# Optimization experiments

Hardware: AMD Instinct MI355X
Metric: run time of the kernel (lower is better)

Reference implementation:

```python
import jax, jax.numpy as jnp
import numpy as np

B, S, IN_DIM, HID = 128, 512, 512, 1024


def setup_inputs() -> dict:
    key = jax.random.key(0)
    k0, k1, k2, k3, k4 = jax.random.split(key, 5)
    s_ih = 1.0 / np.sqrt(HID)
    return {
        "embedding_sequence": jax.random.normal(k0, (B, S, IN_DIM), dtype=jnp.float32),
        "w_ih": jax.random.uniform(k1, (3 * HID, IN_DIM), jnp.float32, -s_ih, s_ih),
        "w_hh": jax.random.uniform(k2, (3 * HID, HID), jnp.float32, -s_ih, s_ih),
        "b_ih": jax.random.uniform(k3, (3 * HID,), jnp.float32, -s_ih, s_ih),
        "b_hh": jax.random.uniform(k4, (3 * HID,), jnp.float32, -s_ih, s_ih),
    }


def _gru_scan(embedding_sequence, w_ih, w_hh, b_ih, b_hh):
    # Precompute input-side gate projections for all steps: [B,S,3H]
    gi_all = jnp.einsum('bsi,gi->bsg', embedding_sequence, w_ih) + b_ih

    def step(h, gi):
        gh = h @ w_hh.T + b_hh                      # [B,3H]
        i_r, i_z, i_n = jnp.split(gi, 3, axis=-1)
        h_r, h_z, h_n = jnp.split(gh, 3, axis=-1)
        r = jax.nn.sigmoid(i_r + h_r)
        z = jax.nn.sigmoid(i_z + h_z)
        n = jnp.tanh(i_n + r * h_n)
        h_new = (1.0 - z) * n + z * h
        return h_new, h_new

    h0 = jnp.zeros((embedding_sequence.shape[0], HID), dtype=embedding_sequence.dtype)
    h_last, hiddens = jax.lax.scan(step, h0, jnp.swapaxes(gi_all, 0, 1))
    return jnp.swapaxes(hiddens, 0, 1), h_last      # ([B,S,H], [B,H])


def reference(embedding_sequence, w_ih, w_hh, b_ih, b_hh):
    return _gru_scan(embedding_sequence, w_ih, w_hh, b_ih, b_hh)
```

## Files before the change

kernel.cpp:

```cpp
#include <hip/hip_runtime.h>
#include <hip/hip_bf16.h>

#define BB   128
#define SS   512
#define IND  512
#define HID  1024
#define NBLK 256
#define GRPBLK 64
#define NSTRIPE 8

#define WHH_LD (HID + 8)
#define WIH_LD (IND + 8)

typedef __attribute__((ext_vector_type(8))) short s8v;
typedef __attribute__((ext_vector_type(4))) float f4v;
typedef unsigned long long u64;
typedef unsigned int u32;

__device__ __forceinline__ short f2bf(float f) {
    union { float f; u32 u; } v; v.f = f;
    u32 u = v.u + 0x7FFFu + ((v.u >> 16) & 1u);
    return (short)(u >> 16);
}


__global__ void __launch_bounds__(128, 1)
gru_persistent(const float* __restrict__ X,
               const float* __restrict__ Wih,
               const float* __restrict__ Whh,
               const float* __restrict__ bih,
               const float* __restrict__ bhh,
               float* __restrict__ out,
               short* __restrict__ bufA,
               short* __restrict__ bufB,
               u64*   __restrict__ ctr)
{
    __shared__ __align__(16) short whh_lds[48 * WHH_LD];
    __shared__ __align__(16) short wih_lds[48 * WIH_LD];

    const int tid  = threadIdx.x;
    const int wave = tid >> 6;
    const int lane = tid & 63;
    const int blk  = blockIdx.x;
    const int mi   = blk >> 6;
    const int jg   = blk & 63;

    for (int idx = tid; idx < 48 * (HID / 4); idx += 128) {
        int s = idx / (HID / 4), k4 = idx % (HID / 4);
        int grow = (s >> 4) * HID + jg * 16 + (s & 15);
        float4 v = *(const float4*)(Whh + (size_t)grow * HID + k4 * 4);
        short* d = &whh_lds[s * WHH_LD + k4 * 4];
        d[0] = f2bf(v.x); d[1] = f2bf(v.y); d[2] = f2bf(v.z); d[3] = f2bf(v.w);
    }
    for (int idx = tid; idx < 48 * (IND / 4); idx += 128) {
        int s = idx / (IND / 4), k4 = idx % (IND / 4);
        int grow = (s >> 4) * HID + jg * 16 + (s & 15);
        float4 v = *(const float4*)(Wih + (size_t)grow * IND + k4 * 4);
        short* d = &wih_lds[s * WIH_LD + k4 * 4];
        d[0] = f2bf(v.x); d[1] = f2bf(v.y); d[2] = f2bf(v.z); d[3] = f2bf(v.w);
    }

    const int n  = lane & 15;
    const int kg = lane >> 4;
    const int j  = jg * 16 + n;
    const float bir = bih[j], biz = bih[HID + j], bin_ = bih[2 * HID + j];
    const float bhr = bhh[j], bhz = bhh[HID + j], bhn  = bhh[2 * HID + j];

    const int rowbase = mi * 32 + wave * 16;
    const int wg      = mi * 2 + wave;

    const int wkk = j >> 5, wkg = (j >> 3) & 3;
    const u32 rest   = (u32)wkk * 1024u + (u32)wkg * 256u
                     + (u32)kg * 64u + ((u32)(n & 7) << 1);
    const u32 wbyteA = (u32)wg * 32768u + rest;
    const u32 wbyteB = (u32)mi * 131072u + (u32)(wg & 1) * 32768u + rest;

    const u64* hbA = (const u64*)bufA + (size_t)wg * 4096 + lane * 2;
    const u64* hbB = (const u64*)bufB + (size_t)mi * 16384
                   + (size_t)(wg & 1) * 4096 + lane * 2;

    float hkeep[4] = {0.f, 0.f, 0.f, 0.f};

    __syncthreads();

    for (int t = 0; t < SS; ++t) {
        f4v acc_r  = {0.f,0.f,0.f,0.f};
        f4v acc_z  = {0.f,0.f,0.f,0.f};
        f4v acc_in = {0.f,0.f,0.f,0.f};
        f4v acc_hn = {0.f,0.f,0.f,0.f};

        {
            const float* xrow = X + ((size_t)(rowbase + n) * SS + t) * IND;
            #pragma unroll 4
            for (int kk = 0; kk < IND / 32; ++kk) {
                const int k0 = kk * 32 + kg * 8;
                const float4* px = (const float4*)(xrow + k0);
                float4 x0 = px[0], x1 = px[1];
                s8v a;
                a[0]=f2bf(x0.x); a[1]=f2bf(x0.y); a[2]=f2bf(x0.z); a[3]=f2bf(x0.w);
                a[4]=f2bf(x1.x); a[5]=f2bf(x1.y); a[6]=f2bf(x1.z); a[7]=f2bf(x1.w);
                s8v br = *(const s8v*)&wih_lds[(0 * 16 + n) * WIH_LD + k0];
                s8v bz = *(const s8v*)&wih_lds[(1 * 16 + n) * WIH_LD + k0];
                s8v bn = *(const s8v*)&wih_lds[(2 * 16 + n) * WIH_LD + k0];
                acc_r  = __builtin_amdgcn_mfma_f32_16x16x32_bf16(a, br, acc_r,  0,0,0);
                acc_z  = __builtin_amdgcn_mfma_f32_16x16x32_bf16(a, bz, acc_z,  0,0,0);
                acc_in = __builtin_amdgcn_mfma_f32_16x16x32_bf16(a, bn, acc_in, 0,0,0);
            }
        }

        if (t > 0) {
            const u64* hb = (t & 1) ? hbA : hbB;
            s8v areg[32];
            #pragma unroll
            for (int kk = 0; kk < 32; ++kk) {
                u64 lo = __hip_atomic_load(hb + kk * 128,
                                           __ATOMIC_RELAXED, __HIP_MEMORY_SCOPE_AGENT);
                u64 hi = __hip_atomic_load(hb + kk * 128 + 1,
                                           __ATOMIC_RELAXED, __HIP_MEMORY_SCOPE_AGENT);
                union { u64 q[2]; s8v v; } u; u.q[0] = lo; u.q[1] = hi;
                areg[kk] = u.v;
            }
            #pragma unroll
            for (int kk = 0; kk < 32; ++kk) {
                const int k0 = kk * 32 + kg * 8;
                s8v br = *(const s8v*)&whh_lds[(0 * 16 + n) * WHH_LD + k0];
                s8v bz = *(const s8v*)&whh_lds[(1 * 16 + n) * WHH_LD + k0];
                s8v bn = *(const s8v*)&whh_lds[(2 * 16 + n) * WHH_LD + k0];
                acc_r  = __builtin_amdgcn_mfma_f32_16x16x32_bf16(areg[kk], br, acc_r,  0,0,0);
                acc_z  = __builtin_amdgcn_mfma_f32_16x16x32_bf16(areg[kk], bz, acc_z,  0,0,0);
                acc_hn = __builtin_amdgcn_mfma_f32_16x16x32_bf16(areg[kk], bn, acc_hn, 0,0,0);
            }
        }

        u32 packv[4];
        #pragma unroll
        for (int r = 0; r < 4; ++r) {
            const int b = rowbase + kg * 4 + r;
            float gr = acc_r[r] + bir + bhr;
            float gz = acc_z[r] + biz + bhz;
            float rr = 1.f / (1.f + __expf(-gr));
            float zz = 1.f / (1.f + __expf(-gz));
            float hn = acc_hn[r] + bhn;
            float na = acc_in[r] + bin_ + rr * hn;
            float e2 = __expf(2.f * na);
            float nn = (e2 - 1.f) / (e2 + 1.f);
            float hnew = (1.f - zz) * nn + zz * hkeep[r];
            hkeep[r] = hnew;
            out[(size_t)b * (SS * HID) + (size_t)t * HID + j] = hnew;
            if (t == SS - 1)
                out[(size_t)BB * SS * HID + (size_t)b * HID + j] = hnew;
            u32 hb16  = (u32)(unsigned short)f2bf(hnew);
            u32 other = (u32)__shfl_xor((int)hb16, 1);
            packv[r] = hb16 | (other << 16);
        }

        if (t < SS - 1) {
            if (!(n & 1)) {
                char* base = (t & 1) ? ((char*)bufB + wbyteB) : ((char*)bufA + wbyteA);
                #pragma unroll
                for (int r = 0; r < 4; ++r)
                    __hip_atomic_store((u32*)(base + r * 16), packv[r],
                                       __ATOMIC_RELAXED, __HIP_MEMORY_SCOPE_AGENT);
            }
            __syncthreads();
            if (tid == 0) {
                __hip_atomic_fetch_add(&ctr[(mi * NSTRIPE + (blk & 7)) * 8], 1ull,
                                       __ATOMIC_RELAXED, __HIP_MEMORY_SCOPE_AGENT);
                const u64 target = (u64)GRPBLK * (u64)(t + 1);
                for (;;) {
                    u64 s = 0;
                    #pragma unroll
                    for (int i = 0; i < NSTRIPE; ++i)
                        s += __hip_atomic_load(&ctr[(mi * NSTRIPE + i) * 8],
                                               __ATOMIC_RELAXED,
                                               __HIP_MEMORY_SCOPE_AGENT);
                    if (s >= target) break;
                    __builtin_amdgcn_s_sleep(1);
                }
            }
            __syncthreads();
        }
    }
}

extern "C" void kernel_launch(void* const* d_in, const int* in_sizes, int n_in,
                              void* d_out, int out_size, void* d_ws, size_t ws_size,
                              hipStream_t stream) {
    const float* X   = (const float*)d_in[0];
    const float* Wih = (const float*)d_in[1];
    const float* Whh = (const float*)d_in[2];
    const float* bih = (const float*)d_in[3];
    const float* bhh = (const float*)d_in[4];
    float* out = (float*)d_out;

    u64*   ctr  = (u64*)d_ws;
    short* bufA = (short*)((char*)d_ws + 4096);
    short* bufB = (short*)(out + (size_t)BB * SS * HID);

    hipMemsetAsync(d_ws, 0, 4096, stream);

    void* args[] = { (void*)&X, (void*)&Wih, (void*)&Whh, (void*)&bih,
                     (void*)&bhh, (void*)&out, (void*)&bufA, (void*)&bufB,
                     (void*)&ctr };
    hipLaunchCooperativeKernel((const void*)gru_persistent,
                               dim3(NBLK), dim3(128), args, 0, stream);
}
```

Baseline: 4.069 ms.

## Split GRU gate matmuls across six waves with LDS reduction

The block grows from 2 to 6 waves, and each wave group handles one gate (r, z, n) instead of one wave computing all three. Gate results are gathered through a small LDS buffer, and wave group 0 applies the nonlinearity and publishes h. Hidden-state loads are also issued before the input projection so their latency is hidden. This shortens the serial MFMA chain per step on the recurrent critical path, at the cost of an extra block barrier, LDS traffic, and redundant h loads in three waves.

```diff
diff --git a/kernel.cpp b/kernel.cpp
--- a/kernel.cpp
+++ b/kernel.cpp
@@ -8,6 +8,7 @@
 #define NBLK 256
 #define GRPBLK 64
 #define NSTRIPE 8
+#define NTHR 384
 
 #define WHH_LD (HID + 8)
 #define WIH_LD (IND + 8)
@@ -24,7 +25,7 @@
 }
 
 
-__global__ void __launch_bounds__(128, 1)
+__global__ void __launch_bounds__(NTHR, 1)
 gru_persistent(const float* __restrict__ X,
                const float* __restrict__ Wih,
                const float* __restrict__ Whh,
@@ -37,6 +38,7 @@
 {
     __shared__ __align__(16) short whh_lds[48 * WHH_LD];
     __shared__ __align__(16) short wih_lds[48 * WIH_LD];
+    __shared__ __align__(16) f4v  red_lds[3][2][64];
 
     const int tid  = threadIdx.x;
     const int wave = tid >> 6;
@@ -45,14 +47,17 @@
     const int mi   = blk >> 6;
     const int jg   = blk & 63;
 
-    for (int idx = tid; idx < 48 * (HID / 4); idx += 128) {
+    const int g  = wave >> 1;
+    const int rw = wave & 1;
+
+    for (int idx = tid; idx < 48 * (HID / 4); idx += NTHR) {
         int s = idx / (HID / 4), k4 = idx % (HID / 4);
         int grow = (s >> 4) * HID + jg * 16 + (s & 15);
         float4 v = *(const float4*)(Whh + (size_t)grow * HID + k4 * 4);
         short* d = &whh_lds[s * WHH_LD + k4 * 4];
         d[0] = f2bf(v.x); d[1] = f2bf(v.y); d[2] = f2bf(v.z); d[3] = f2bf(v.w);
     }
-    for (int idx = tid; idx < 48 * (IND / 4); idx += 128) {
+    for (int idx = tid; idx < 48 * (IND / 4); idx += NTHR) {
         int s = idx / (IND / 4), k4 = idx % (IND / 4);
         int grow = (s >> 4) * HID + jg * 16 + (s & 15);
         float4 v = *(const float4*)(Wih + (size_t)grow * IND + k4 * 4);
@@ -66,8 +71,8 @@
     const float bir = bih[j], biz = bih[HID + j], bin_ = bih[2 * HID + j];
     const float bhr = bhh[j], bhz = bhh[HID + j], bhn  = bhh[2 * HID + j];
 
-    const int rowbase = mi * 32 + wave * 16;
-    const int wg      = mi * 2 + wave;
+    const int rowbase = mi * 32 + rw * 16;
+    const int wg      = mi * 2 + rw;
 
     const int wkk = j >> 5, wkg = (j >> 3) & 3;
     const u32 rest   = (u32)wkk * 1024u + (u32)wkg * 256u
@@ -84,10 +89,23 @@
     __syncthreads();
 
     for (int t = 0; t < SS; ++t) {
-        f4v acc_r  = {0.f,0.f,0.f,0.f};
-        f4v acc_z  = {0.f,0.f,0.f,0.f};
-        f4v acc_in = {0.f,0.f,0.f,0.f};
-        f4v acc_hn = {0.f,0.f,0.f,0.f};
+        f4v acc_a = {0.f,0.f,0.f,0.f};
+        f4v acc_b = {0.f,0.f,0.f,0.f};
+        s8v areg[32];
+
+        if (t > 0) {
+            const u64* hb = (t & 1) ? hbA : hbB;
+            #pragma unroll
+            for (int kk = 0; kk < 32; ++kk) {
+                u64 lo = __hip_atomic_load(hb + kk * 128,
+                                           __ATOMIC_RELAXED, __HIP_MEMORY_SCOPE_AGENT);
+                u64 hi = __hip_atomic_load(hb + kk * 128 + 1,
+                                           __ATOMIC_RELAXED, __HIP_MEMORY_SCOPE_AGENT);
+                union { u64 q[2]; s8v v; } u; u.q[0] = lo; u.q[1] = hi;
+                areg[kk] = u.v;
+            }
+        }
+        __builtin_amdgcn_sched_barrier(0);
 
         {
             const float* xrow = X + ((size_t)(rowbase + n) * SS + t) * IND;
@@ -99,69 +117,74 @@
                 s8v a;
                 a[0]=f2bf(x0.x); a[1]=f2bf(x0.y); a[2]=f2bf(x0.z); a[3]=f2bf(x0.w);
                 a[4]=f2bf(x1.x); a[5]=f2bf(x1.y); a[6]=f2bf(x1.z); a[7]=f2bf(x1.w);
-                s8v br = *(const s8v*)&wih_lds[(0 * 16 + n) * WIH_LD + k0];
-                s8v bz = *(const s8v*)&wih_lds[(1 * 16 + n) * WIH_LD + k0];
-                s8v bn = *(const s8v*)&wih_lds[(2 * 16 + n) * WIH_LD + k0];
-                acc_r  = __builtin_amdgcn_mfma_f32_16x16x32_bf16(a, br, acc_r,  0,0,0);
-                acc_z  = __builtin_amdgcn_mfma_f32_16x16x32_bf16(a, bz, acc_z,  0,0,0);
-                acc_in = __builtin_amdgcn_mfma_f32_16x16x32_bf16(a, bn, acc_in, 0,0,0);
+                s8v bfrag = *(const s8v*)&wih_lds[(g * 16 + n) * WIH_LD + k0];
+                acc_a = __builtin_amdgcn_mfma_f32_16x16x32_bf16(a, bfrag, acc_a, 0,0,0);
             }
         }
 
         if (t > 0) {
-            const u64* hb = (t & 1) ? hbA : hbB;
-            s8v areg[32];
+            if (g < 2) {
+                #pragma unroll
+                for (int kk = 0; kk < 32; ++kk) {
+                    const int k0 = kk * 32 + kg * 8;
+                    s8v bfrag = *(const s8v*)&whh_lds[(g * 16 + n) * WHH_LD + k0];
+                    acc_a = __builtin_amdgcn_mfma_f32_16x16x32_bf16(areg[kk], bfrag, acc_a, 0,0,0);
+                }
+            } else {
+                #pragma unroll
+                for (int kk = 0; kk < 32; ++kk) {
+                    const int k0 = kk * 32 + kg * 8;
+                    s8v bfrag = *(const s8v*)&whh_lds[(2 * 16 + n) * WHH_LD + k0];
+                    acc_b = __builtin_amdgcn_mfma_f32_16x16x32_bf16(areg[kk], bfrag, acc_b, 0,0,0);
+                }
+            }
+        }
+
+        if (g == 1) {
+            red_lds[0][rw][lane] = acc_a;
+        } else if (g == 2) {
+            red_lds[1][rw][lane] = acc_a;
+            red_lds[2][rw][lane] = acc_b;
+        }
+        __syncthreads();
+
+        if (g == 0) {
+            const f4v acc_r  = acc_a;
+            const f4v acc_z  = red_lds[0][rw][lane];
+            const f4v acc_in = red_lds[1][rw][lane];
+            const f4v acc_hn = red_lds[2][rw][lane];
+
+            u32 packv[4];
             #pragma unroll
-            for (int kk = 0; kk < 32; ++kk) {
-                u64 lo = __hip_atomic_load(hb + kk * 128,
-                                           __ATOMIC_RELAXED, __HIP_MEMORY_SCOPE_AGENT);
-                u64 hi = __hip_atomic_load(hb + kk * 128 + 1,
-                                           __ATOMIC_RELAXED, __HIP_MEMORY_SCOPE_AGENT);
-                union { u64 q[2]; s8v v; } u; u.q[0] = lo; u.q[1] = hi;
-                areg[kk] = u.v;
-            }
-            #pragma unroll
-            for (int kk = 0; kk < 32; ++kk) {
-                const int k0 = kk * 32 + kg * 8;
-                s8v br = *(const s8v*)&whh_lds[(0 * 16 + n) * WHH_LD + k0];
-                s8v bz = *(const s8v*)&whh_lds[(1 * 16 + n) * WHH_LD + k0];
-                s8v bn = *(const s8v*)&whh_lds[(2 * 16 + n) * WHH_LD + k0];
-                acc_r  = __builtin_amdgcn_mfma_f32_16x16x32_bf16(areg[kk], br, acc_r,  0,0,0);
-                acc_z  = __builtin_amdgcn_mfma_f32_16x16x32_bf16(areg[kk], bz, acc_z,  0,0,0);
-                acc_hn = __builtin_amdgcn_mfma_f32_16x16x32_bf16(areg[kk], bn, acc_hn, 0,0,0);
-            }
-        }
-
-        u32 packv[4];
-        #pragma unroll
-        for (int r = 0; r < 4; ++r) {
-            const int b = rowbase + kg * 4 + r;
-            float gr = acc_r[r] + bir + bhr;
-            float gz = acc_z[r] + biz + bhz;
-            float rr = 1.f / (1.f + __expf(-gr));
-            float zz = 1.f / (1.f + __expf(-gz));
-            float hn = acc_hn[r] + bhn;
-            float na = acc_in[r] + bin_ + rr * hn;
-            float e2 = __expf(2.f * na);
-            float nn = (e2 - 1.f) / (e2 + 1.f);
-            float hnew = (1.f - zz) * nn + zz * hkeep[r];
-            hkeep[r] = hnew;
-            out[(size_t)b * (SS * HID) + (size_t)t * HID + j] = hnew;
-            if (t == SS - 1)
-                out[(size_t)BB * SS * HID + (size_t)b * HID + j] = hnew;
-            u32 hb16  = (u32)(unsigned short)f2bf(hnew);
-            u32 other = (u32)__shfl_xor((int)hb16, 1);
-            packv[r] = hb16 | (other << 16);
-        }
-
-        if (t < SS - 1) {
-            if (!(n & 1)) {
+            for (int r = 0; r < 4; ++r) {
+                const int b = rowbase + kg * 4 + r;
+                float gr = acc_r[r] + bir + bhr;
+                float gz = acc_z[r] + biz + bhz;
+                float rr = 1.f / (1.f + __expf(-gr));
+                float zz = 1.f / (1.f + __expf(-gz));
+                float hn = acc_hn[r] + bhn;
+                float na = acc_in[r] + bin_ + rr * hn;
+                float e2 = __expf(2.f * na);
+                float nn = (e2 - 1.f) / (e2 + 1.f);
+                float hnew = (1.f - zz) * nn + zz * hkeep[r];
+                hkeep[r] = hnew;
+                out[(size_t)b * (SS * HID) + (size_t)t * HID + j] = hnew;
+                if (t == SS - 1)
+                    out[(size_t)BB * SS * HID + (size_t)b * HID + j] = hnew;
+                u32 hb16  = (u32)(unsigned short)f2bf(hnew);
+                u32 other = (u32)__shfl_xor((int)hb16, 1);
+                packv[r] = hb16 | (other << 16);
+            }
+            if (t < SS - 1 && !(n & 1)) {
                 char* base = (t & 1) ? ((char*)bufB + wbyteB) : ((char*)bufA + wbyteA);
                 #pragma unroll
                 for (int r = 0; r < 4; ++r)
                     __hip_atomic_store((u32*)(base + r * 16), packv[r],
                                        __ATOMIC_RELAXED, __HIP_MEMORY_SCOPE_AGENT);
             }
+        }
+
+        if (t < SS - 1) {
             __syncthreads();
             if (tid == 0) {
                 __hip_atomic_fetch_add(&ctr[(mi * NSTRIPE + (blk & 7)) * 8], 1ull,
@@ -203,5 +226,5 @@
                      (void*)&bhh, (void*)&out, (void*)&bufA, (void*)&bufB,
                      (void*)&ctr };
     hipLaunchCooperativeKernel((const void*)gru_persistent,
-                               dim3(NBLK), dim3(128), args, 0, stream);
+                               dim3(NBLK), dim3(NTHR), args, 0, stream);
 }
```

After: 7.428 ms. 1.83x slower.

## Add producer waves precomputing next-step input projections in a double-buffered LDS ring

Applied to the files above, without the earlier changes.

Doubles the block to four waves. Two producer waves compute the input-side gate projection X_t·W_ih for step t+1 into a double-buffered LDS array, while two consumer waves do the recurrent h·W_hh matmul and the gate math for step t. This takes the input projection off the serial per-step critical path. In exchange it adds wave-level role specialization and LDS traffic, and the per-step barrier now also waits for the producer waves.

```diff
diff --git a/kernel.cpp b/kernel.cpp
--- a/kernel.cpp
+++ b/kernel.cpp
@@ -8,6 +8,7 @@
 #define NBLK 256
 #define GRPBLK 64
 #define NSTRIPE 8
+#define NTHR 256
 
 #define WHH_LD (HID + 8)
 #define WIH_LD (IND + 8)
@@ -24,7 +25,7 @@
 }
 
 
-__global__ void __launch_bounds__(128, 1)
+__global__ void __launch_bounds__(NTHR, 1)
 gru_persistent(const float* __restrict__ X,
                const float* __restrict__ Wih,
                const float* __restrict__ Whh,
@@ -37,6 +38,7 @@
 {
     __shared__ __align__(16) short whh_lds[48 * WHH_LD];
     __shared__ __align__(16) short wih_lds[48 * WIH_LD];
+    __shared__ __align__(16) f4v  gibuf[2][3][2][64];
 
     const int tid  = threadIdx.x;
     const int wave = tid >> 6;
@@ -45,14 +47,17 @@
     const int mi   = blk >> 6;
     const int jg   = blk & 63;
 
-    for (int idx = tid; idx < 48 * (HID / 4); idx += 128) {
+    const int consumer = (wave < 2);
+    const int rw = wave & 1;
+
+    for (int idx = tid; idx < 48 * (HID / 4); idx += NTHR) {
         int s = idx / (HID / 4), k4 = idx % (HID / 4);
         int grow = (s >> 4) * HID + jg * 16 + (s & 15);
         float4 v = *(const float4*)(Whh + (size_t)grow * HID + k4 * 4);
         short* d = &whh_lds[s * WHH_LD + k4 * 4];
         d[0] = f2bf(v.x); d[1] = f2bf(v.y); d[2] = f2bf(v.z); d[3] = f2bf(v.w);
     }
-    for (int idx = tid; idx < 48 * (IND / 4); idx += 128) {
+    for (int idx = tid; idx < 48 * (IND / 4); idx += NTHR) {
         int s = idx / (IND / 4), k4 = idx % (IND / 4);
         int grow = (s >> 4) * HID + jg * 16 + (s & 15);
         float4 v = *(const float4*)(Wih + (size_t)grow * IND + k4 * 4);
@@ -66,8 +71,8 @@
     const float bir = bih[j], biz = bih[HID + j], bin_ = bih[2 * HID + j];
     const float bhr = bhh[j], bhz = bhh[HID + j], bhn  = bhh[2 * HID + j];
 
-    const int rowbase = mi * 32 + wave * 16;
-    const int wg      = mi * 2 + wave;
+    const int rowbase = mi * 32 + rw * 16;
+    const int wg      = mi * 2 + rw;
 
     const int wkk = j >> 5, wkg = (j >> 3) & 3;
     const u32 rest   = (u32)wkk * 1024u + (u32)wkg * 256u
@@ -83,14 +88,94 @@
 
     __syncthreads();
 
+    if (!consumer) {
+        f4v gr = {0.f,0.f,0.f,0.f}, gz = gr, gn = gr;
+        const float* xrow = X + ((size_t)(rowbase + n) * SS + 0) * IND;
+        #pragma unroll 4
+        for (int kk = 0; kk < IND / 32; ++kk) {
+            const int k0 = kk * 32 + kg * 8;
+            const float4* px = (const float4*)(xrow + k0);
+            float4 x0 = px[0], x1 = px[1];
+            s8v a;
+            a[0]=f2bf(x0.x); a[1]=f2bf(x0.y); a[2]=f2bf(x0.z); a[3]=f2bf(x0.w);
+            a[4]=f2bf(x1.x); a[5]=f2bf(x1.y); a[6]=f2bf(x1.z); a[7]=f2bf(x1.w);
+            s8v br = *(const s8v*)&wih_lds[(0 * 16 + n) * WIH_LD + k0];
+            s8v bz = *(const s8v*)&wih_lds[(1 * 16 + n) * WIH_LD + k0];
+            s8v bn = *(const s8v*)&wih_lds[(2 * 16 + n) * WIH_LD + k0];
+            gr = __builtin_amdgcn_mfma_f32_16x16x32_bf16(a, br, gr, 0,0,0);
+            gz = __builtin_amdgcn_mfma_f32_16x16x32_bf16(a, bz, gz, 0,0,0);
+            gn = __builtin_amdgcn_mfma_f32_16x16x32_bf16(a, bn, gn, 0,0,0);
+        }
+        gibuf[0][0][rw][lane] = gr;
+        gibuf[0][1][rw][lane] = gz;
+        gibuf[0][2][rw][lane] = gn;
+    }
+    __syncthreads();
+
     for (int t = 0; t < SS; ++t) {
-        f4v acc_r  = {0.f,0.f,0.f,0.f};
-        f4v acc_z  = {0.f,0.f,0.f,0.f};
-        f4v acc_in = {0.f,0.f,0.f,0.f};
-        f4v acc_hn = {0.f,0.f,0.f,0.f};
-
-        {
-            const float* xrow = X + ((size_t)(rowbase + n) * SS + t) * IND;
+        if (consumer) {
+            s8v areg[32];
+            if (t > 0) {
+                const u64* hb = (t & 1) ? hbA : hbB;
+                #pragma unroll
+                for (int kk = 0; kk < 32; ++kk) {
+                    u64 lo = __hip_atomic_load(hb + kk * 128,
+                                               __ATOMIC_RELAXED, __HIP_MEMORY_SCOPE_AGENT);
+                    u64 hi = __hip_atomic_load(hb + kk * 128 + 1,
+                                               __ATOMIC_RELAXED, __HIP_MEMORY_SCOPE_AGENT);
+                    union { u64 q[2]; s8v v; } u; u.q[0] = lo; u.q[1] = hi;
+                    areg[kk] = u.v;
+                }
+            }
+            f4v acc_r  = gibuf[t & 1][0][rw][lane];
+            f4v acc_z  = gibuf[t & 1][1][rw][lane];
+            f4v acc_in = gibuf[t & 1][2][rw][lane];
+            f4v acc_hn = {0.f,0.f,0.f,0.f};
+
+            if (t > 0) {
+                #pragma unroll
+                for (int kk = 0; kk < 32; ++kk) {
+                    const int k0 = kk * 32 + kg * 8;
+                    s8v br = *(const s8v*)&whh_lds[(0 * 16 + n) * WHH_LD + k0];
+                    s8v bz = *(const s8v*)&whh_lds[(1 * 16 + n) * WHH_LD + k0];
+                    s8v bn = *(const s8v*)&whh_lds[(2 * 16 + n) * WHH_LD + k0];
+                    acc_r  = __builtin_amdgcn_mfma_f32_16x16x32_bf16(areg[kk], br, acc_r,  0,0,0);
+                    acc_z  = __builtin_amdgcn_mfma_f32_16x16x32_bf16(areg[kk], bz, acc_z,  0,0,0);
+                    acc_hn = __builtin_amdgcn_mfma_f32_16x16x32_bf16(areg[kk], bn, acc_hn, 0,0,0);
+                }
+            }
+
+            u32 packv[4];
+            #pragma unroll
+            for (int r = 0; r < 4; ++r) {
+                const int b = rowbase + kg * 4 + r;
+                float gr = acc_r[r] + bir + bhr;
+                float gz = acc_z[r] + biz + bhz;
+                float rr = 1.f / (1.f + __expf(-gr));
+                float zz = 1.f / (1.f + __expf(-gz));
+                float hn = acc_hn[r] + bhn;
+                float na = acc_in[r] + bin_ + rr * hn;
+                float e2 = __expf(2.f * na);
+                float nn = (e2 - 1.f) / (e2 + 1.f);
+                float hnew = (1.f - zz) * nn + zz * hkeep[r];
+                hkeep[r] = hnew;
+                out[(size_t)b * (SS * HID) + (size_t)t * HID + j] = hnew;
+                if (t == SS - 1)
+                    out[(size_t)BB * SS * HID + (size_t)b * HID + j] = hnew;
+                u32 hb16  = (u32)(unsigned short)f2bf(hnew);
+                u32 other = (u32)__shfl_xor((int)hb16, 1);
+                packv[r] = hb16 | (other << 16);
+            }
+            if (t < SS - 1 && !(n & 1)) {
+                char* base = (t & 1) ? ((char*)bufB + wbyteB) : ((char*)bufA + wbyteA);
+                #pragma unroll
+                for (int r = 0; r < 4; ++r)
+                    __hip_atomic_store((u32*)(base + r * 16), packv[r],
+                                       __ATOMIC_RELAXED, __HIP_MEMORY_SCOPE_AGENT);
+            }
+        } else if (t < SS - 1) {
+            f4v gr = {0.f,0.f,0.f,0.f}, gz = gr, gn = gr;
+            const float* xrow = X + ((size_t)(rowbase + n) * SS + (t + 1)) * IND;
             #pragma unroll 4
             for (int kk = 0; kk < IND / 32; ++kk) {
                 const int k0 = kk * 32 + kg * 8;
@@ -102,66 +187,16 @@
                 s8v br = *(const s8v*)&wih_lds[(0 * 16 + n) * WIH_LD + k0];
                 s8v bz = *(const s8v*)&wih_lds[(1 * 16 + n) * WIH_LD + k0];
                 s8v bn = *(const s8v*)&wih_lds[(2 * 16 + n) * WIH_LD + k0];
-                acc_r  = __builtin_amdgcn_mfma_f32_16x16x32_bf16(a, br, acc_r,  0,0,0);
-                acc_z  = __builtin_amdgcn_mfma_f32_16x16x32_bf16(a, bz, acc_z,  0,0,0);
-                acc_in = __builtin_amdgcn_mfma_f32_16x16x32_bf16(a, bn, acc_in, 0,0,0);
-            }
+                gr = __builtin_amdgcn_mfma_f32_16x16x32_bf16(a, br, gr, 0,0,0);
+                gz = __builtin_amdgcn_mfma_f32_16x16x32_bf16(a, bz, gz, 0,0,0);
+                gn = __builtin_amdgcn_mfma_f32_16x16x32_bf16(a, bn, gn, 0,0,0);
+            }
+            gibuf[(t + 1) & 1][0][rw][lane] = gr;
+            gibuf[(t + 1) & 1][1][rw][lane] = gz;
+            gibuf[(t + 1) & 1][2][rw][lane] = gn;
         }
 
-        if (t > 0) {
-            const u64* hb = (t & 1) ? hbA : hbB;
-            s8v areg[32];
-            #pragma unroll
-            for (int kk = 0; kk < 32; ++kk) {
-                u64 lo = __hip_atomic_load(hb + kk * 128,
-                                           __ATOMIC_RELAXED, __HIP_MEMORY_SCOPE_AGENT);
-                u64 hi = __hip_atomic_load(hb + kk * 128 + 1,
-                                           __ATOMIC_RELAXED, __HIP_MEMORY_SCOPE_AGENT);
-                union { u64 q[2]; s8v v; } u; u.q[0] = lo; u.q[1] = hi;
-                areg[kk] = u.v;
-            }
-            #pragma unroll
-            for (int kk = 0; kk < 32; ++kk) {
-                const int k0 = kk * 32 + kg * 8;
-                s8v br = *(const s8v*)&whh_lds[(0 * 16 + n) * WHH_LD + k0];
-                s8v bz = *(const s8v*)&whh_lds[(1 * 16 + n) * WHH_LD + k0];
-                s8v bn = *(const s8v*)&whh_lds[(2 * 16 + n) * WHH_LD + k0];
-                acc_r  = __builtin_amdgcn_mfma_f32_16x16x32_bf16(areg[kk], br, acc_r,  0,0,0);
-                acc_z  = __builtin_amdgcn_mfma_f32_16x16x32_bf16(areg[kk], bz, acc_z,  0,0,0);
-                acc_hn = __builtin_amdgcn_mfma_f32_16x16x32_bf16(areg[kk], bn, acc_hn, 0,0,0);
-            }
-        }
-
-        u32 packv[4];
-        #pragma unroll
-        for (int r = 0; r < 4; ++r) {
-            const int b = rowbase + kg * 4 + r;
-            float gr = acc_r[r] + bir + bhr;
-            float gz = acc_z[r] + biz + bhz;
-            float rr = 1.f / (1.f + __expf(-gr));
-            float zz = 1.f / (1.f + __expf(-gz));
-            float hn = acc_hn[r] + bhn;
-            float na = acc_in[r] + bin_ + rr * hn;
-            float e2 = __expf(2.f * na);
-            float nn = (e2 - 1.f) / (e2 + 1.f);
-            float hnew = (1.f - zz) * nn + zz * hkeep[r];
-            hkeep[r] = hnew;
-            out[(size_t)b * (SS * HID) + (size_t)t * HID + j] = hnew;
-            if (t == SS - 1)
-                out[(size_t)BB * SS * HID + (size_t)b * HID + j] = hnew;
-            u32 hb16  = (u32)(unsigned short)f2bf(hnew);
-            u32 other = (u32)__shfl_xor((int)hb16, 1);
-            packv[r] = hb16 | (other << 16);
-        }
-
         if (t < SS - 1) {
-            if (!(n & 1)) {
-                char* base = (t & 1) ? ((char*)bufB + wbyteB) : ((char*)bufA + wbyteA);
-                #pragma unroll
-                for (int r = 0; r < 4; ++r)
-                    __hip_atomic_store((u32*)(base + r * 16), packv[r],
-                                       __ATOMIC_RELAXED, __HIP_MEMORY_SCOPE_AGENT);
-            }
             __syncthreads();
             if (tid == 0) {
                 __hip_atomic_fetch_add(&ctr[(mi * NSTRIPE + (blk & 7)) * 8], 1ull,
@@ -203,5 +238,5 @@
                      (void*)&bhh, (void*)&out, (void*)&bufA, (void*)&bufB,
                      (void*)&ctr };
     hipLaunchCooperativeKernel((const void*)gru_persistent,
-                               dim3(NBLK), dim3(128), args, 0, stream);
+                               dim3(NBLK), dim3(NTHR), args, 0, stream);
 }
```

Result: slower. 5.475 ms (+34.6%).
